# Kernel optimization log

Measured on AMD Instinct MI355X. Metric: run time of the kernel, lower is better.

Reference implementation:

```python
import jax, jax.numpy as jnp
import numpy as np


def setup_inputs() -> dict:
    key = jax.random.key(0)
    k1, k2 = jax.random.split(key)
    twoE, d, n = 1600000, 4, 50000
    maps = jax.random.normal(k1, (twoE, d, d), dtype=jnp.float32)
    edge_index = jax.random.randint(k2, (2, twoE), 0, n, dtype=jnp.int64 if jax.config.jax_enable_x64 else jnp.int32)
    return {"maps": maps, "edge_index": edge_index, "num_nodes": n}


def reference(maps, edge_index, num_nodes):
    # maps: [2E, d, d], edge_index: [2, 2E]
    n = num_nodes
    d = maps.shape[1]
    E = maps.shape[0] // 2
    row = edge_index[0, :E]
    col = edge_index[1, :E]
    left_maps = maps[:E]
    right_maps = maps[E:]

    # diag_contrib[e] = maps[e]^T @ maps[e]
    diag_contrib = jnp.einsum('eab,eac->ebc', maps, maps)
    maps_diag = jnp.zeros((n, d, d), dtype=maps.dtype).at[edge_index[0]].add(diag_contrib)
    # off-diagonal blocks: left^T @ right
    maps_triu = jnp.einsum('eab,eac->ebc', left_maps, right_maps)

    # cartesian_prod(arange(d), arange(d)) -> [d*d, 2]
    a = jnp.arange(d)
    grid = jnp.stack(jnp.meshgrid(a, a, indexing='ij'), axis=-1).reshape(-1, 2)

    # diagonal blocks: offsets (i*d, i*d)
    node_off = (jnp.arange(n) * d)[:, None]                      # [n,1]
    diag_idx = grid[None] + jnp.concatenate([node_off, node_off], axis=1)[:, None, :]  # [n,d*d,2]
    diag_vals = maps_diag.reshape(n * d * d)

    # off-diagonal blocks -maps_triu at (i,j) and its transpose at (j,i)
    off_ij = jnp.stack([row * d, col * d], axis=1)[:, None, :]   # [E,1,2]
    off_ji = jnp.stack([col * d, row * d], axis=1)[:, None, :]
    idx_ij = grid[None] + off_ij                                  # [E,d*d,2]
    idx_ji = grid[None] + off_ji
    vals_ij = (-maps_triu).reshape(E * d * d)
    vals_ji = (-jnp.swapaxes(maps_triu, 1, 2)).reshape(E * d * d)

    indices = jnp.concatenate([diag_idx.reshape(-1, 2), idx_ij.reshape(-1, 2), idx_ji.reshape(-1, 2)], axis=0).T  # [2,M]
    values = jnp.concatenate([diag_vals, vals_ij, vals_ji], axis=0)

    # emulate COO coalesce ordering (row-major sort; assumes simple graph -> no duplicate entries)
    order = jnp.lexsort((indices[1], indices[0]))
    return indices[:, order], values[order]
```

## Files before the change

kernel.cpp:

```cpp
#include <hip/hip_runtime.h>
#include <stdint.h>

#define THREADS 256
#define N_MAX 131072
#define B_MAX 2100000

__device__ int g_cnt[N_MAX];
__device__ int g_cnt2[N_MAX];
__device__ int g_blk_off[N_MAX + 1];
__device__ int g_off2[N_MAX + 1];
__device__ float g_maps_diag[(size_t)N_MAX * 16];
__device__ unsigned long long g_keys[B_MAX];
__device__ int g_perm[B_MAX];
__device__ int g_wide;

__device__ __forceinline__ int get_ei(const int* __restrict__ ei, int wide, long long idx) {
  return ei[idx << wide];
}

__device__ __forceinline__ unsigned long long shfl_xor_u64(unsigned long long x, int mask) {
  int lo = (int)(x & 0xFFFFFFFFULL);
  int hi = (int)(x >> 32);
  lo = __shfl_xor(lo, mask, 64);
  hi = __shfl_xor(hi, mask, 64);
  return ((unsigned long long)(unsigned int)hi << 32) | (unsigned int)lo;
}

__global__ void hist_kernel(const int* __restrict__ ei, int E, int twoE) {
  __shared__ int s_w;
  if (threadIdx.x == 0) {
    int w = 1;
    int lim = (twoE >= 8) ? 8 : twoE;
    for (int i = 0; i < lim; i++)
      if (ei[2 * i + 1] != 0) w = 0;
    s_w = w;
    if (blockIdx.x == 0) g_wide = w;
  }
  __syncthreads();
  int w = s_w;
  int g = blockIdx.x * blockDim.x + threadIdx.x;
  if (g >= twoE) return;
  int a0 = get_ei(ei, w, g);
  atomicAdd(&g_cnt2[a0], 1);
  if (g < E) {
    atomicAdd(&g_cnt[a0], 1);
    atomicAdd(&g_cnt[get_ei(ei, w, (long long)twoE + g)], 1);
  }
}

__global__ void scan_kernel(int n) {
  __shared__ int partial[1024];
  int which = blockIdx.x;
  int tid = threadIdx.x;
  int chunk = (n + 1023) / 1024;
  int start = tid * chunk;
  int end = min(start + chunk, n);
  int add1 = (which == 0) ? 1 : 0;
  const int* src = (which == 0) ? g_cnt : g_cnt2;
  int* dst = (which == 0) ? g_blk_off : g_off2;
  int s = 0;
  for (int u = start; u < end; u++) s += src[u] + add1;
  partial[tid] = s;
  __syncthreads();
  for (int off = 1; off < 1024; off <<= 1) {
    int v = (tid >= off) ? partial[tid - off] : 0;
    __syncthreads();
    partial[tid] += v;
    __syncthreads();
  }
  int run = (tid == 0) ? 0 : partial[tid - 1];
  for (int u = start; u < end; u++) { dst[u] = run; run += src[u] + add1; }
  if (tid == 1023) dst[n] = partial[1023];
}

__global__ void scatter_fill_kernel(const int* __restrict__ ei, int E, int twoE) {
  int g = blockIdx.x * blockDim.x + threadIdx.x;
  if (g >= twoE) return;
  int w = g_wide;
  int u = get_ei(ei, w, g);
  int p = g_off2[u] + atomicSub(&g_cnt2[u], 1) - 1;
  g_perm[p] = g;
  if (g < E) {
    int v = get_ei(ei, w, (long long)twoE + g);
    int c1 = atomicSub(&g_cnt[u], 1);
    int p1 = g_blk_off[u] + c1;
    g_keys[p1] = ((unsigned long long)u << 44) | ((unsigned long long)v << 22) |
                 (1ULL << 20) | (unsigned long long)g;
    int c2 = atomicSub(&g_cnt[v], 1);
    int p2 = g_blk_off[v] + c2;
    g_keys[p2] = ((unsigned long long)v << 44) | ((unsigned long long)u << 22) |
                 (2ULL << 20) | (unsigned long long)g;
  }
}

__global__ void diag_place_kernel(const float* __restrict__ maps, int n) {
  int t = blockIdx.x * blockDim.x + threadIdx.x;
  int u = t >> 2;
  int h = t & 3;
  if (u >= n) return;
  int s = g_off2[u];
  int epos = g_off2[u + 1];
  float acc[10];
#pragma unroll
  for (int i = 0; i < 10; i++) acc[i] = 0.0f;
  for (int i = s + h; i < epos; i += 4) {
    int g = g_perm[i];
    const float4* Mv = reinterpret_cast<const float4*>(maps + (size_t)g * 16);
    float4 t0 = Mv[0], t1 = Mv[1], t2 = Mv[2], t3 = Mv[3];
    float m[16] = {t0.x, t0.y, t0.z, t0.w, t1.x, t1.y, t1.z, t1.w,
                   t2.x, t2.y, t2.z, t2.w, t3.x, t3.y, t3.z, t3.w};
    int p = 0;
#pragma unroll
    for (int a = 0; a < 4; a++)
#pragma unroll
      for (int b = a; b < 4; b++) {
        acc[p] += m[0 + a] * m[0 + b] + m[4 + a] * m[4 + b] + m[8 + a] * m[8 + b] + m[12 + a] * m[12 + b];
        p++;
      }
  }
#pragma unroll
  for (int i = 0; i < 10; i++) {
    acc[i] += __shfl_xor(acc[i], 1, 64);
    acc[i] += __shfl_xor(acc[i], 2, 64);
  }
  if (h == 0) {
    float d[16];
    int p = 0;
#pragma unroll
    for (int a = 0; a < 4; a++)
#pragma unroll
      for (int b = a; b < 4; b++) {
        d[a * 4 + b] = acc[p];
        d[b * 4 + a] = acc[p];
        p++;
      }
    float4* D = reinterpret_cast<float4*>(g_maps_diag + (size_t)u * 16);
#pragma unroll
    for (int i = 0; i < 4; i++) D[i] = make_float4(d[4 * i], d[4 * i + 1], d[4 * i + 2], d[4 * i + 3]);
    int pp = g_blk_off[u];
    g_keys[pp] = ((unsigned long long)u << 44) | ((unsigned long long)u << 22);
  }
}

__global__ __launch_bounds__(256) void sort_kernel(int n) {
  int wv = (blockIdx.x * blockDim.x + threadIdx.x) >> 6;
  int lane = threadIdx.x & 63;
  if (wv >= n) return;
  int s = g_blk_off[wv];
  int c = g_blk_off[wv + 1] - s;
  if (c <= 1) return;
  if (c <= 64) {
    unsigned long long k = (lane < c) ? g_keys[s + lane] : ~0ULL;
    for (int kk = 2; kk <= 64; kk <<= 1) {
      for (int j = kk >> 1; j > 0; j >>= 1) {
        unsigned long long o = shfl_xor_u64(k, j);
        bool tm = ((lane & j) == 0) == ((lane & kk) == 0);
        unsigned long long lo = (k < o) ? k : o;
        unsigned long long hi = (k < o) ? o : k;
        k = tm ? lo : hi;
      }
    }
    if (lane < c) g_keys[s + lane] = k;
  } else if (c <= 128) {
    unsigned long long k0 = (lane < c) ? g_keys[s + lane] : ~0ULL;
    unsigned long long k1 = (lane + 64 < c) ? g_keys[s + lane + 64] : ~0ULL;
    for (int kk = 2; kk <= 128; kk <<= 1) {
      for (int j = kk >> 1; j > 0; j >>= 1) {
        if (j == 64) {
          unsigned long long lo = (k0 < k1) ? k0 : k1;
          unsigned long long hi = (k0 < k1) ? k1 : k0;
          k0 = lo; k1 = hi;
        } else {
          unsigned long long o0 = shfl_xor_u64(k0, j);
          unsigned long long o1 = shfl_xor_u64(k1, j);
          bool jb = ((lane & j) == 0);
          bool tm0 = jb == ((lane & kk) == 0);
          bool tm1 = jb == (((lane + 64) & kk) == 0);
          unsigned long long lo0 = (k0 < o0) ? k0 : o0;
          unsigned long long hi0 = (k0 < o0) ? o0 : k0;
          unsigned long long lo1 = (k1 < o1) ? k1 : o1;
          unsigned long long hi1 = (k1 < o1) ? o1 : k1;
          k0 = tm0 ? lo0 : hi0;
          k1 = tm1 ? lo1 : hi1;
        }
      }
    }
    if (lane < c) g_keys[s + lane] = k0;
    if (lane + 64 < c) g_keys[s + lane + 64] = k1;
  } else {
    if (lane == 0) {
      for (int i = s + 1; i < s + c; i++) {
        unsigned long long kk2 = g_keys[i];
        int j = i - 1;
        while (j >= s && g_keys[j] > kk2) { g_keys[j + 1] = g_keys[j]; j--; }
        g_keys[j + 1] = kk2;
      }
    }
  }
}

__global__ void emit_kernel(const float* __restrict__ maps, int E, long long T, int totalBlocks,
                            float* __restrict__ out) {
  int idx = blockIdx.x * blockDim.x + threadIdx.x;
  if (idx >= totalBlocks) return;
  unsigned long long key = g_keys[idx];
  int u = (int)(key >> 44);
  int base = g_blk_off[u];
  int cntu = g_blk_off[u + 1] - base;
  int k = idx - base;
  int v = (int)((key >> 22) & 0x3FFFFFULL);
  int cls = (int)((key >> 20) & 3ULL);
  int e = (int)(key & 0xFFFFFULL);
  unsigned long long vtag = key >> 22;

  int k0 = k;
  while (k0 > 0 && (g_keys[base + k0 - 1] >> 22) == vtag) k0--;
  int k1 = k;
  while (k1 + 1 < cntu && (g_keys[base + k1 + 1] >> 22) == vtag) k1++;
  int m = k1 - k0 + 1;
  int j = k - k0;

  float val[16];
  if (cls == 0) {
    const float* D = g_maps_diag + (size_t)u * 16;
#pragma unroll
    for (int i = 0; i < 16; i++) val[i] = D[i];
  } else {
    const float* L = maps + (size_t)e * 16;
    const float* R = maps + ((size_t)E + (size_t)e) * 16;
    float l[16], r[16];
#pragma unroll
    for (int i = 0; i < 16; i++) { l[i] = L[i]; r[i] = R[i]; }
    if (cls == 1) {
#pragma unroll
      for (int a = 0; a < 4; a++)
#pragma unroll
        for (int b = 0; b < 4; b++)
          val[a * 4 + b] = -(l[0 + a] * r[0 + b] + l[4 + a] * r[4 + b] + l[8 + a] * r[8 + b] + l[12 + a] * r[12 + b]);
    } else {
#pragma unroll
      for (int a = 0; a < 4; a++)
#pragma unroll
        for (int b = 0; b < 4; b++)
          val[a * 4 + b] = -(l[0 + b] * r[0 + a] + l[4 + b] * r[4 + a] + l[8 + b] * r[8 + a] + l[12 + b] * r[12 + a]);
    }
  }

  float* orow = out;
  float* ocol = out + T;
  float* oval = out + 2 * T;
  long long blkbase = 16LL * base + 4LL * k0;
  float cf = (float)(v * 4);
#pragma unroll
  for (int a = 0; a < 4; a++) {
    long long rowbase = blkbase + (long long)a * 4 * cntu;
    float rf = (float)(u * 4 + a);
    if (m == 1) {
      *reinterpret_cast<float4*>(orow + rowbase) = make_float4(rf, rf, rf, rf);
      *reinterpret_cast<float4*>(ocol + rowbase) = make_float4(cf, cf + 1.0f, cf + 2.0f, cf + 3.0f);
      *reinterpret_cast<float4*>(oval + rowbase) =
          make_float4(val[a * 4 + 0], val[a * 4 + 1], val[a * 4 + 2], val[a * 4 + 3]);
    } else {
#pragma unroll
      for (int b = 0; b < 4; b++) {
        long long pos = rowbase + (long long)b * m + j;
        orow[pos] = rf;
        ocol[pos] = cf + (float)b;
        oval[pos] = val[a * 4 + b];
      }
    }
  }
}

extern "C" void kernel_launch(void* const* d_in, const int* in_sizes, int n_in,
                              void* d_out, int out_size, void* d_ws, size_t ws_size,
                              hipStream_t stream) {
  const float* maps = (const float*)d_in[0];
  const int* ei = (const int*)d_in[1];

  long long twoE = (long long)in_sizes[1] / 2;
  long long E = twoE / 2;
  long long T = (long long)out_size / 3;
  long long totalBlocks = T / 16;
  long long n = totalBlocks - twoE;
  if (n < 1 || n > N_MAX || totalBlocks > B_MAX || twoE > B_MAX) return;

  int iE = (int)E, i2E = (int)twoE, iN = (int)n, iB = (int)totalBlocks;
  int g2E = (i2E + THREADS - 1) / THREADS;
  int gD = (4 * iN + THREADS - 1) / THREADS;
  int gSort = (iN + 3) / 4;
  int gB = (iB + THREADS - 1) / THREADS;

  hist_kernel<<<g2E, THREADS, 0, stream>>>(ei, iE, i2E);
  scan_kernel<<<2, 1024, 0, stream>>>(iN);
  scatter_fill_kernel<<<g2E, THREADS, 0, stream>>>(ei, iE, i2E);
  diag_place_kernel<<<gD, THREADS, 0, stream>>>(maps, iN);
  sort_kernel<<<gSort, 256, 0, stream>>>(iN);
  emit_kernel<<<gB, THREADS, 0, stream>>>(maps, iE, T, iB, (float*)d_out);
}
```

Before: 910.3 us.

## Pack edge counters into one word and reuse sorted keys for diagonal accumulation

Merges the two per-node count arrays into a single packed int (high 16 bits for block counts, low 16 for second-half diag contributions), so each edge does fewer atomics and the scan reads one array. The diagonal kernel now takes first-half edge contributions from the already bucketed key array and only uses a smaller permutation for second-half edges. It also widens the per-node thread group from 4 to 8 lanes. The 16-bit packing risks overflow on high-degree nodes and adds branchy key decoding in the diagonal loop.

```diff
diff --git a/kernel.cpp b/kernel.cpp
--- a/kernel.cpp
+++ b/kernel.cpp
@@ -5,13 +5,12 @@
 #define N_MAX 131072
 #define B_MAX 2100000
 
-__device__ int g_cnt[N_MAX];
-__device__ int g_cnt2[N_MAX];
+__device__ int g_packed[N_MAX];
 __device__ int g_blk_off[N_MAX + 1];
 __device__ int g_off2[N_MAX + 1];
 __device__ float g_maps_diag[(size_t)N_MAX * 16];
 __device__ unsigned long long g_keys[B_MAX];
-__device__ int g_perm[B_MAX];
+__device__ int g_perm2[B_MAX];
 __device__ int g_wide;
 
 __device__ __forceinline__ int get_ei(const int* __restrict__ ei, int wide, long long idx) {
@@ -40,11 +39,12 @@
   int w = s_w;
   int g = blockIdx.x * blockDim.x + threadIdx.x;
   if (g >= twoE) return;
-  int a0 = get_ei(ei, w, g);
-  atomicAdd(&g_cnt2[a0], 1);
+  int s0 = get_ei(ei, w, g);
   if (g < E) {
-    atomicAdd(&g_cnt[a0], 1);
-    atomicAdd(&g_cnt[get_ei(ei, w, (long long)twoE + g)], 1);
+    atomicAdd(&g_packed[s0], 1 << 16);
+    atomicAdd(&g_packed[get_ei(ei, w, (long long)twoE + g)], 1 << 16);
+  } else {
+    atomicAdd(&g_packed[s0], 1);
   }
 }
 
@@ -55,11 +55,12 @@
   int chunk = (n + 1023) / 1024;
   int start = tid * chunk;
   int end = min(start + chunk, n);
-  int add1 = (which == 0) ? 1 : 0;
-  const int* src = (which == 0) ? g_cnt : g_cnt2;
   int* dst = (which == 0) ? g_blk_off : g_off2;
   int s = 0;
-  for (int u = start; u < end; u++) s += src[u] + add1;
+  for (int u = start; u < end; u++) {
+    int pk = g_packed[u];
+    s += (which == 0) ? (int)(((unsigned)pk) >> 16) + 1 : (pk & 0xFFFF);
+  }
   partial[tid] = s;
   __syncthreads();
   for (int off = 1; off < 1024; off <<= 1) {
@@ -69,7 +70,11 @@
     __syncthreads();
   }
   int run = (tid == 0) ? 0 : partial[tid - 1];
-  for (int u = start; u < end; u++) { dst[u] = run; run += src[u] + add1; }
+  for (int u = start; u < end; u++) {
+    dst[u] = run;
+    int pk = g_packed[u];
+    run += (which == 0) ? (int)(((unsigned)pk) >> 16) + 1 : (pk & 0xFFFF);
+  }
   if (tid == 1023) dst[n] = partial[1023];
 }
 
@@ -77,34 +82,59 @@
   int g = blockIdx.x * blockDim.x + threadIdx.x;
   if (g >= twoE) return;
   int w = g_wide;
-  int u = get_ei(ei, w, g);
-  int p = g_off2[u] + atomicSub(&g_cnt2[u], 1) - 1;
-  g_perm[p] = g;
   if (g < E) {
+    int u = get_ei(ei, w, g);
     int v = get_ei(ei, w, (long long)twoE + g);
-    int c1 = atomicSub(&g_cnt[u], 1);
-    int p1 = g_blk_off[u] + c1;
-    g_keys[p1] = ((unsigned long long)u << 44) | ((unsigned long long)v << 22) |
-                 (1ULL << 20) | (unsigned long long)g;
-    int c2 = atomicSub(&g_cnt[v], 1);
-    int p2 = g_blk_off[v] + c2;
-    g_keys[p2] = ((unsigned long long)v << 44) | ((unsigned long long)u << 22) |
-                 (2ULL << 20) | (unsigned long long)g;
+    int old = atomicSub(&g_packed[u], 1 << 16);
+    int h = (int)(((unsigned)old) >> 16);
+    g_keys[g_blk_off[u] + h] = ((unsigned long long)u << 44) | ((unsigned long long)v << 22) |
+                               (1ULL << 20) | (unsigned long long)g;
+  } else {
+    int e = g - E;
+    int s2 = get_ei(ei, w, g);
+    int ue = get_ei(ei, w, (long long)twoE + e);
+    int ve = get_ei(ei, w, e);
+    int old1 = atomicSub(&g_packed[ue], 1 << 16);
+    int old2 = atomicSub(&g_packed[s2], 1);
+    int h1 = (int)(((unsigned)old1) >> 16);
+    g_keys[g_blk_off[ue] + h1] = ((unsigned long long)ue << 44) | ((unsigned long long)ve << 22) |
+                                 (2ULL << 20) | (unsigned long long)e;
+    g_perm2[g_off2[s2] + (old2 & 0xFFFF) - 1] = g;
   }
 }
 
 __global__ void diag_place_kernel(const float* __restrict__ maps, int n) {
   int t = blockIdx.x * blockDim.x + threadIdx.x;
-  int u = t >> 2;
-  int h = t & 3;
+  int u = t >> 3;
+  int h = t & 7;
   if (u >= n) return;
-  int s = g_off2[u];
-  int epos = g_off2[u + 1];
+  int kb = g_blk_off[u];
+  int ke = g_blk_off[u + 1];
   float acc[10];
 #pragma unroll
   for (int i = 0; i < 10; i++) acc[i] = 0.0f;
-  for (int i = s + h; i < epos; i += 4) {
-    int g = g_perm[i];
+  for (int i = kb + 1 + h; i < ke; i += 8) {
+    unsigned long long key = g_keys[i];
+    if (((key >> 20) & 3ULL) == 1ULL) {
+      int e = (int)(key & 0xFFFFFULL);
+      const float4* Mv = reinterpret_cast<const float4*>(maps + (size_t)e * 16);
+      float4 t0 = Mv[0], t1 = Mv[1], t2 = Mv[2], t3 = Mv[3];
+      float m[16] = {t0.x, t0.y, t0.z, t0.w, t1.x, t1.y, t1.z, t1.w,
+                     t2.x, t2.y, t2.z, t2.w, t3.x, t3.y, t3.z, t3.w};
+      int p = 0;
+#pragma unroll
+      for (int a = 0; a < 4; a++)
+#pragma unroll
+        for (int b = a; b < 4; b++) {
+          acc[p] += m[0 + a] * m[0 + b] + m[4 + a] * m[4 + b] + m[8 + a] * m[8 + b] + m[12 + a] * m[12 + b];
+          p++;
+        }
+    }
+  }
+  int s2 = g_off2[u];
+  int e2 = g_off2[u + 1];
+  for (int i = s2 + h; i < e2; i += 8) {
+    int g = g_perm2[i];
     const float4* Mv = reinterpret_cast<const float4*>(maps + (size_t)g * 16);
     float4 t0 = Mv[0], t1 = Mv[1], t2 = Mv[2], t3 = Mv[3];
     float m[16] = {t0.x, t0.y, t0.z, t0.w, t1.x, t1.y, t1.z, t1.w,
@@ -122,6 +152,7 @@
   for (int i = 0; i < 10; i++) {
     acc[i] += __shfl_xor(acc[i], 1, 64);
     acc[i] += __shfl_xor(acc[i], 2, 64);
+    acc[i] += __shfl_xor(acc[i], 4, 64);
   }
   if (h == 0) {
     float d[16];
@@ -137,8 +168,7 @@
     float4* D = reinterpret_cast<float4*>(g_maps_diag + (size_t)u * 16);
 #pragma unroll
     for (int i = 0; i < 4; i++) D[i] = make_float4(d[4 * i], d[4 * i + 1], d[4 * i + 2], d[4 * i + 3]);
-    int pp = g_blk_off[u];
-    g_keys[pp] = ((unsigned long long)u << 44) | ((unsigned long long)u << 22);
+    g_keys[kb] = ((unsigned long long)u << 44) | ((unsigned long long)u << 22);
   }
 }
 
@@ -287,7 +317,7 @@
 
   int iE = (int)E, i2E = (int)twoE, iN = (int)n, iB = (int)totalBlocks;
   int g2E = (i2E + THREADS - 1) / THREADS;
-  int gD = (4 * iN + THREADS - 1) / THREADS;
+  int gD = (8 * iN + THREADS - 1) / THREADS;
   int gSort = (iN + 3) / 4;
   int gB = (iB + THREADS - 1) / THREADS;
 
```

After: 877.9 us. 1.04x faster.
